# Optimization experiments

Measured on AMD Instinct MI355X. Metric: run time of the kernel, lower is better.

The kernel has to match this reference:

```python
import jax, jax.numpy as jnp
import numpy as np

EMBED = 2048
N_HEAD = 32
N_KV = 8
HEAD_DIM = 64
GROUP = N_HEAD // N_KV


def _rope_tables(seq_len, head_dim):
    inv_freq = 1.0 / (10000.0 ** (jnp.arange(0, head_dim, 2, dtype=jnp.float32) / head_dim))
    ang = jnp.arange(seq_len, dtype=jnp.float32)[:, None] * inv_freq[None, :]  # [S, D/2]
    ang = jnp.concatenate([ang, ang], axis=-1)  # [S, D]
    return jnp.cos(ang), jnp.sin(ang)


def apply_rope(x, cos, sin, offset=0):
    # x: [B, H, S, D]
    S, D = x.shape[2], x.shape[3]
    x1, x2 = x[..., : D // 2], x[..., D // 2 :]
    c = cos[offset : offset + S][None, None]
    s = sin[offset : offset + S][None, None]
    rotated = jnp.concatenate([-x2, x1], axis=-1)
    return (x * c + rotated * s).astype(x.dtype)


def setup_inputs() -> dict:
    key = jax.random.key(0)
    kx, kq, kk, kv, ko = jax.random.split(key, 5)
    B, S = 2, 2048
    x = jax.random.normal(kx, (B, S, EMBED), dtype=jnp.float32)
    mask = jnp.triu(jnp.ones((S, S), dtype=bool), k=1)  # causal: True = masked
    cos, sin = _rope_tables(S, HEAD_DIM)
    std = 0.02
    Wq = jax.random.normal(kq, (EMBED, EMBED), dtype=jnp.float32) * std
    Wk = jax.random.normal(kk, (EMBED, N_KV * HEAD_DIM), dtype=jnp.float32) * std
    Wv = jax.random.normal(kv, (EMBED, N_KV * HEAD_DIM), dtype=jnp.float32) * std
    Wo = jax.random.normal(ko, (EMBED, EMBED), dtype=jnp.float32) * std
    return {"x": x, "mask": mask, "cos": cos, "sin": sin,
            "Wq": Wq, "Wk": Wk, "Wv": Wv, "Wo": Wo}


def reference(x, mask, cos, sin, Wq, Wk, Wv, Wo):
    B, S, E = x.shape
    # projections (no bias)
    q = (x @ Wq).reshape(B, S, N_HEAD, HEAD_DIM).transpose(0, 2, 1, 3)  # [B,H,S,D]
    k = (x @ Wk).reshape(B, S, N_KV, HEAD_DIM).transpose(0, 2, 1, 3)    # [B,G,S,D]
    v = (x @ Wv).reshape(B, S, N_KV, HEAD_DIM).transpose(0, 2, 1, 3)    # [B,G,S,D]
    q = apply_rope(q, cos, sin, offset=0)
    k = apply_rope(k, cos, sin, offset=0)
    next_k, next_v = k, v  # kv cache to return
    # GQA: head h uses kv group h // GROUP; avoid repeat_interleave via reshape
    qg = q.reshape(B, N_KV, GROUP, S, HEAD_DIM)
    scores = jnp.einsum('bgjsd,bgtd->bgjst', qg, k) / np.float32(np.sqrt(HEAD_DIM))
    scores = jnp.where(mask[None, None, None], -jnp.inf, scores)
    attn = jax.nn.softmax(scores, axis=-1)
    out = jnp.einsum('bgjst,bgtd->bgjsd', attn, v)          # [B,G,group,S,D]
    out = out.reshape(B, N_HEAD, S, HEAD_DIM).transpose(0, 2, 1, 3).reshape(B, S, E)
    return out @ Wo, next_k, next_v
```

## Files before the change

kernel.cpp:

```cpp
#include <hip/hip_runtime.h>
#include <hip/hip_bf16.h>
#include <math.h>

#define NH 32
#define NKV 8
#define HD 64
#define B_ 2
#define S_ 2048
#define E_ 2048
#define M_ 4096

typedef unsigned short ushort_t;
typedef __attribute__((ext_vector_type(8))) short short8;
typedef __attribute__((ext_vector_type(4))) short short4v;
typedef __attribute__((ext_vector_type(4))) float floatx4;

__device__ inline unsigned short f2bf(float f) {
  unsigned int u = __float_as_uint(f);
  return (unsigned short)((u + 0x7FFFu + ((u >> 16) & 1u)) >> 16);
}

__device__ inline float fexp2(float x) {
  float r;
  asm("v_exp_f32 %0, %1" : "=v"(r) : "v"(x));
  return r;
}

__device__ inline void ld_lds16(const void* g, void* l) {
  __builtin_amdgcn_global_load_lds((__attribute__((address_space(1))) void*)g,
                                   (__attribute__((address_space(3))) void*)l, 16, 0, 0);
}

__global__ __launch_bounds__(256) void cast_x(const float* __restrict__ x,
                                              ushort_t* __restrict__ xb) {
  size_t i = ((size_t)blockIdx.x * 256 + threadIdx.x) * 8;
  float4 a = *(const float4*)(x + i);
  float4 b = *(const float4*)(x + i + 4);
  short8 o;
  o[0] = (short)f2bf(a.x); o[1] = (short)f2bf(a.y);
  o[2] = (short)f2bf(a.z); o[3] = (short)f2bf(a.w);
  o[4] = (short)f2bf(b.x); o[5] = (short)f2bf(b.y);
  o[6] = (short)f2bf(b.z); o[7] = (short)f2bf(b.w);
  *(short8*)(xb + i) = o;
}

__global__ __launch_bounds__(256) void transpose_w(const float* __restrict__ in,
                                                   ushort_t* __restrict__ out,
                                                   int R, int C) {
  __shared__ float tile[32][33];
  int c0 = blockIdx.x * 32, r0 = blockIdx.y * 32;
  int x = threadIdx.x, y0 = threadIdx.y;
  for (int i = 0; i < 4; i++) {
    int r = y0 + i * 8;
    tile[r][x] = in[(size_t)(r0 + r) * C + c0 + x];
  }
  __syncthreads();
  for (int i = 0; i < 4; i++) {
    int r = y0 + i * 8;
    out[(size_t)(c0 + r) * R + r0 + x] = f2bf(tile[x][r]);
  }
}

__global__ __launch_bounds__(256) void transpose_v(const float* __restrict__ outv,
                                                   ushort_t* __restrict__ vt) {
  __shared__ float t64[64][65];
  int bg = blockIdx.y;
  int tt = blockIdx.x;
  int s0 = tt * 64;
  int tid = threadIdx.x;
  size_t ibase = (size_t)bg * S_ * HD + (size_t)s0 * HD;
  for (int i = tid; i < 1024; i += 256) {
    int sr = i >> 4, dc = (i & 15) * 4;
    float4 v = *(const float4*)(outv + ibase + (size_t)sr * HD + dc);
    t64[sr][dc] = v.x; t64[sr][dc + 1] = v.y; t64[sr][dc + 2] = v.z; t64[sr][dc + 3] = v.w;
  }
  __syncthreads();
  size_t obase = ((size_t)bg * 32 + tt) * 4096;
  for (int i = tid; i < 512; i += 256) {
    int d = i >> 3, ss = (i & 7) * 8;
    short8 o;
#pragma unroll
    for (int e = 0; e < 8; e++) o[e] = (short)f2bf(t64[ss + e][d]);
    *(short8*)(vt + obase + d * 64 + (ss ^ ((d & 7) << 3))) = o;
  }
}

__global__ __launch_bounds__(256) void gemm_qkv(const ushort_t* __restrict__ xb,
                                                const ushort_t* __restrict__ WT,
                                                ushort_t* __restrict__ qbf,
                                                float* __restrict__ outk,
                                                ushort_t* __restrict__ kbf,
                                                float* __restrict__ outv,
                                                const float* __restrict__ cosP,
                                                const float* __restrict__ sinP) {
  __shared__ __align__(16) ushort_t As[128][32];
  __shared__ __align__(16) ushort_t Bs[128][32];
  const int K = 2048;
  int tid = threadIdx.x;
  int m0 = blockIdx.y * 128, n0 = blockIdx.x * 128;
  int w = tid >> 6, lane = tid & 63;
  int wm = (w >> 1) * 64, wn = (w & 1) * 64;
  int lr = lane & 15, quad = lane >> 4;
  int srow = lane >> 2, soff = (lane & 3) * 16;
  floatx4 acc[4][4] = {};
  for (int kt = 0; kt < 64; kt++) {
    __syncthreads();
#pragma unroll
    for (int j = 0; j < 2; j++) {
      int r = j * 64 + w * 16;
      ld_lds16((const char*)(xb + (size_t)(m0 + r + srow) * K) + kt * 64 + soff,
               (char*)As + r * 64);
      ld_lds16((const char*)(WT + (size_t)(n0 + r + srow) * K) + kt * 64 + soff,
               (char*)Bs + r * 64);
    }
    __syncthreads();
    short8 af[4], bf[4];
#pragma unroll
    for (int i = 0; i < 4; i++) af[i] = *(const short8*)(&As[wm + i * 16 + lr][quad * 8]);
#pragma unroll
    for (int j = 0; j < 4; j++) bf[j] = *(const short8*)(&Bs[wn + j * 16 + lr][quad * 8]);
#pragma unroll
    for (int i = 0; i < 4; i++)
#pragma unroll
      for (int j = 0; j < 4; j++)
        acc[i][j] = __builtin_amdgcn_mfma_f32_16x16x32_bf16(af[i], bf[j], acc[i][j], 0, 0, 0);
  }
  if (n0 < 2048) {
    const float QS = 0.125f * 1.4426950408889634f;
#pragma unroll
    for (int i = 0; i < 4; i++)
#pragma unroll
      for (int j = 0; j < 2; j++) {
        int d = j * 16 + lr;
#pragma unroll
        for (int r = 0; r < 4; r++) {
          int row = m0 + wm + i * 16 + quad * 4 + r;
          int s = row & (S_ - 1);
          float c = cosP[s * 64 + d], sn = sinP[s * 64 + d];
          float x1 = acc[i][j][r], x2 = acc[i][j + 2][r];
          size_t o = (size_t)row * 2048 + n0 + wn + d;
          qbf[o] = f2bf((x1 * c - x2 * sn) * QS);
          qbf[o + 32] = f2bf((x2 * c + x1 * sn) * QS);
        }
      }
  } else if (n0 < 2560) {
    int h = (n0 - 2048 + wn) >> 6;
#pragma unroll
    for (int i = 0; i < 4; i++)
#pragma unroll
      for (int j = 0; j < 2; j++) {
        int d = j * 16 + lr;
#pragma unroll
        for (int r = 0; r < 4; r++) {
          int row = m0 + wm + i * 16 + quad * 4 + r;
          int s = row & (S_ - 1), b = row >> 11;
          float c = cosP[s * 64 + d], sn = sinP[s * 64 + d];
          float x1 = acc[i][j][r], x2 = acc[i][j + 2][r];
          float y1 = x1 * c - x2 * sn, y2 = x2 * c + x1 * sn;
          size_t rowb = ((size_t)(b * NKV + h) * S_ + s) * 64;
          int xr = (s & 7) << 3;
          outk[rowb + d] = y1; outk[rowb + d + 32] = y2;
          kbf[rowb + (d ^ xr)] = f2bf(y1);
          kbf[rowb + ((d + 32) ^ xr)] = f2bf(y2);
        }
      }
  } else {
    int cv0 = n0 - 2560 + wn;
    int h = cv0 >> 6;
#pragma unroll
    for (int i = 0; i < 4; i++)
#pragma unroll
      for (int j = 0; j < 4; j++) {
        int d = j * 16 + lr;
#pragma unroll
        for (int r = 0; r < 4; r++) {
          int row = m0 + wm + i * 16 + quad * 4 + r;
          int s = row & (S_ - 1), b = row >> 11;
          outv[((size_t)(b * NKV + h) * S_ + s) * 64 + d] = acc[i][j][r];
        }
      }
  }
}

__global__ __launch_bounds__(256) void gemm_o(const ushort_t* __restrict__ ctx,
                                              const ushort_t* __restrict__ WoT,
                                              float* __restrict__ y) {
  __shared__ __align__(16) ushort_t As[128][32];
  __shared__ __align__(16) ushort_t Bs[128][32];
  const int K = 2048, N = 2048;
  int tid = threadIdx.x;
  int m0 = blockIdx.y * 128, n0 = blockIdx.x * 128;
  int w = tid >> 6, lane = tid & 63;
  int wm = (w >> 1) * 64, wn = (w & 1) * 64;
  int lr = lane & 15, quad = lane >> 4;
  int srow = lane >> 2, soff = (lane & 3) * 16;
  floatx4 acc[4][4] = {};
  for (int kt = 0; kt < 64; kt++) {
    __syncthreads();
#pragma unroll
    for (int j = 0; j < 2; j++) {
      int r = j * 64 + w * 16;
      ld_lds16((const char*)(ctx + (size_t)(m0 + r + srow) * K) + kt * 64 + soff,
               (char*)As + r * 64);
      ld_lds16((const char*)(WoT + (size_t)(n0 + r + srow) * K) + kt * 64 + soff,
               (char*)Bs + r * 64);
    }
    __syncthreads();
    short8 af[4], bf[4];
#pragma unroll
    for (int i = 0; i < 4; i++) af[i] = *(const short8*)(&As[wm + i * 16 + lr][quad * 8]);
#pragma unroll
    for (int j = 0; j < 4; j++) bf[j] = *(const short8*)(&Bs[wn + j * 16 + lr][quad * 8]);
#pragma unroll
    for (int i = 0; i < 4; i++)
#pragma unroll
      for (int j = 0; j < 4; j++)
        acc[i][j] = __builtin_amdgcn_mfma_f32_16x16x32_bf16(af[i], bf[j], acc[i][j], 0, 0, 0);
  }
#pragma unroll
  for (int i = 0; i < 4; i++)
#pragma unroll
    for (int j = 0; j < 4; j++) {
      int row = m0 + wm + i * 16 + quad * 4;
      int col = n0 + wn + j * 16 + lr;
#pragma unroll
      for (int r = 0; r < 4; r++)
        y[(size_t)(row + r) * N + col] = acc[i][j][r];
    }
}

__global__ __launch_bounds__(256, 4) void attn2(ushort_t* __restrict__ q,
                                                const ushort_t* __restrict__ k,
                                                const ushort_t* __restrict__ vt) {
  __shared__ __align__(16) ushort_t KV[2][2][64][64];
  __shared__ __align__(16) ushort_t Ps[4][16][64];
  int bh = blockIdx.x;
  int qt = 31 - blockIdx.y;
  int b = bh >> 5, h = bh & 31, g = h >> 2;
  int tid = threadIdx.x;
  int w = tid >> 6, lane = tid & 63;
  int lr = lane & 15, quad = lane >> 4;

  int qg = qt * 64 + w * 16 + lr;
  short8 aq0, aq1;
  {
    const ushort_t* qp = q + ((size_t)(b * S_ + qg) * NH + h) * HD;
    aq0 = *(const short8*)(qp + quad * 8);
    aq1 = *(const short8*)(qp + 32 + quad * 8);
  }
  floatx4 od[4] = {};
  float mi = -INFINITY, li = 0.f;

  const char* ksrc = (const char*)(k + (size_t)(b * NKV + g) * S_ * HD) + w * 2048 + lane * 16;
  const char* vsrc = (const char*)(vt + (size_t)(b * NKV + g) * S_ * HD) + w * 2048 + lane * 16;
  char* dB = (char*)&KV[0][0][0][0] + w * 2048;

  int sw = (lr & 7) << 4;
  int ro0 = (quad * 16) ^ sw;
  int ro1 = (64 + quad * 16) ^ sw;
  char* Pw = (char*)&Ps[0][0][0] + w * 2048;

  ld_lds16(ksrc, dB);
  ld_lds16(ksrc + 1024, dB + 1024);
  ld_lds16(vsrc, dB + 8192);
  ld_lds16(vsrc + 1024, dB + 8192 + 1024);
  asm volatile("s_waitcnt vmcnt(0)" ::: "memory");
  __syncthreads();

  int cur = 0;
  for (int t = 0; t <= qt; t++) {
    if (t < qt) {
      const char* kn = ksrc + (size_t)(t + 1) * 8192;
      const char* vn = vsrc + (size_t)(t + 1) * 8192;
      char* d = dB + (cur ^ 1) * 16384;
      ld_lds16(kn, d); ld_lds16(kn + 1024, d + 1024);
      ld_lds16(vn, d + 8192); ld_lds16(vn + 1024, d + 8192 + 1024);
    }
    const char* Kb = (const char*)&KV[cur][0][0][0];
    const char* Vb = (const char*)&KV[cur][1][0][0];
    floatx4 sc[4];
#pragma unroll
    for (int kn = 0; kn < 4; kn++) {
      short8 a0 = *(const short8*)(Kb + (kn * 16 + lr) * 128 + ro0);
      short8 a1 = *(const short8*)(Kb + (kn * 16 + lr) * 128 + ro1);
      floatx4 c = {};
      c = __builtin_amdgcn_mfma_f32_16x16x32_bf16(a0, aq0, c, 0, 0, 0);
      c = __builtin_amdgcn_mfma_f32_16x16x32_bf16(a1, aq1, c, 0, 0, 0);
      sc[kn] = c;
    }
    float pv[16];
#pragma unroll
    for (int kn = 0; kn < 4; kn++)
#pragma unroll
      for (int r = 0; r < 4; r++) pv[kn * 4 + r] = sc[kn][r];
    if (t == qt) {
#pragma unroll
      for (int e = 0; e < 16; e++) {
        int kg = t * 64 + (e >> 2) * 16 + quad * 4 + (e & 3);
        if (kg > qg) pv[e] = -INFINITY;
      }
    }
    float mx = pv[0];
#pragma unroll
    for (int e = 1; e < 16; e++) mx = fmaxf(mx, pv[e]);
    mx = fmaxf(mx, __shfl_xor(mx, 16));
    mx = fmaxf(mx, __shfl_xor(mx, 32));
    if (__any(mx > mi + 11.5f)) {
      float mn = fmaxf(mi, mx);
      float al = fexp2(mi - mn);
      li *= al;
#pragma unroll
      for (int dn = 0; dn < 4; dn++) {
        od[dn][0] *= al; od[dn][1] *= al; od[dn][2] *= al; od[dn][3] *= al;
      }
      mi = mn;
    }
    float ps = 0.f;
#pragma unroll
    for (int e = 0; e < 16; e++) {
      pv[e] = fexp2(pv[e] - mi);
      ps += pv[e];
    }
    ps += __shfl_xor(ps, 16);
    ps += __shfl_xor(ps, 32);
    li += ps;
#pragma unroll
    for (int kn = 0; kn < 4; kn++) {
      unsigned int u0, u1;
      asm("v_cvt_pk_bf16_f32 %0, %1, %2" : "=v"(u0) : "v"(pv[kn * 4 + 0]), "v"(pv[kn * 4 + 1]));
      asm("v_cvt_pk_bf16_f32 %0, %1, %2" : "=v"(u1) : "v"(pv[kn * 4 + 2]), "v"(pv[kn * 4 + 3]));
      uint2 uu; uu.x = u0; uu.y = u1;
      *(uint2*)(Pw + lr * 128 + ((kn * 32 + quad * 8) ^ sw)) = uu;
    }
    short8 pb0 = *(const short8*)(Pw + lr * 128 + ro0);
    short8 pb1 = *(const short8*)(Pw + lr * 128 + ro1);
#pragma unroll
    for (int dn = 0; dn < 4; dn++) {
      short8 va = *(const short8*)(Vb + (dn * 16 + lr) * 128 + ro0);
      short8 vb = *(const short8*)(Vb + (dn * 16 + lr) * 128 + ro1);
      od[dn] = __builtin_amdgcn_mfma_f32_16x16x32_bf16(va, pb0, od[dn], 0, 0, 0);
      od[dn] = __builtin_amdgcn_mfma_f32_16x16x32_bf16(vb, pb1, od[dn], 0, 0, 0);
    }
    asm volatile("s_waitcnt vmcnt(0)" ::: "memory");
    __syncthreads();
    cur ^= 1;
  }
  float inv = 1.f / li;
  ushort_t* outp = q + ((size_t)(b * S_ + qg) * NH + h) * HD;
#pragma unroll
  for (int dn = 0; dn < 4; dn++) {
    short4v u;
    u[0] = (short)f2bf(od[dn][0] * inv); u[1] = (short)f2bf(od[dn][1] * inv);
    u[2] = (short)f2bf(od[dn][2] * inv); u[3] = (short)f2bf(od[dn][3] * inv);
    *(short4v*)(outp + dn * 16 + quad * 4) = u;
  }
}

extern "C" void kernel_launch(void* const* d_in, const int* in_sizes, int n_in,
                              void* d_out, int out_size, void* d_ws, size_t ws_size,
                              hipStream_t stream) {
  const float* x = (const float*)d_in[0];
  const float* cosT = (const float*)d_in[2];
  const float* sinT = (const float*)d_in[3];
  const float* Wq = (const float*)d_in[4];
  const float* Wk = (const float*)d_in[5];
  const float* Wv = (const float*)d_in[6];
  const float* Wo = (const float*)d_in[7];

  char* ws = (char*)d_ws;
  ushort_t* WT = (ushort_t*)(ws);
  ushort_t* WoT = (ushort_t*)(ws + 12582912);
  ushort_t* xb = (ushort_t*)(ws + 20971520);
  ushort_t* qbf = (ushort_t*)(ws + 37748736);
  ushort_t* kbf = (ushort_t*)(ws + 54525952);
  ushort_t* vt = (ushort_t*)(ws + 58720256);

  float* y = (float*)d_out;
  float* outk = y + (size_t)M_ * E_;
  float* outv = outk + (size_t)B_ * NKV * S_ * HD;

  cast_x<<<dim3(4096), 256, 0, stream>>>(x, xb);
  transpose_w<<<dim3(64, 64), dim3(32, 8), 0, stream>>>(Wq, WT, 2048, 2048);
  transpose_w<<<dim3(16, 64), dim3(32, 8), 0, stream>>>(Wk, WT + 2048 * 2048, 2048, 512);
  transpose_w<<<dim3(16, 64), dim3(32, 8), 0, stream>>>(Wv, WT + 2560 * 2048, 2048, 512);
  transpose_w<<<dim3(64, 64), dim3(32, 8), 0, stream>>>(Wo, WoT, 2048, 2048);

  gemm_qkv<<<dim3(24, 32), 256, 0, stream>>>(xb, WT, qbf, outk, kbf, outv, cosT, sinT);
  transpose_v<<<dim3(32, 16), 256, 0, stream>>>(outv, vt);

  attn2<<<dim3(64, 32), 256, 0, stream>>>(qbf, kbf, vt);

  gemm_o<<<dim3(16, 32), 256, 0, stream>>>(qbf, WoT, y);
}
```

Baseline: 360.6 us.

## Double-buffer GEMM tiles with wider K step, XOR-swizzled LDS, and block swizzle

```diff
diff --git a/kernel.cpp b/kernel.cpp
--- a/kernel.cpp
+++ b/kernel.cpp
@@ -85,6 +85,73 @@
   }
 }
 
+__device__ __forceinline__ void gemm128_core(const ushort_t* __restrict__ Ag,
+                                             const ushort_t* __restrict__ Bg,
+                                             floatx4 (&acc)[4][4]) {
+  __shared__ __align__(16) ushort_t As[2][128][64];
+  __shared__ __align__(16) ushort_t Bs[2][128][64];
+  int tid = threadIdx.x;
+  int w = tid >> 6, lane = tid & 63;
+  int wm = (w >> 1) * 64, wn = (w & 1) * 64;
+  int lr = lane & 15, quad = lane >> 4;
+  int sx = lr & 7;
+  char* Asb = (char*)As;
+  char* Bsb = (char*)Bs;
+
+  size_t so[4];
+#pragma unroll
+  for (int s = 0; s < 4; s++)
+    so[s] = (size_t)(w * 32 + s * 8 + (lane >> 3)) * 4096 + (size_t)(((lane & 7) ^ (lane >> 3)) * 16);
+  const char* abase = (const char*)Ag;
+  const char* bbase = (const char*)Bg;
+
+#define STAGE128(buf, kt)                                          \
+  do {                                                             \
+    size_t ko = (size_t)(kt) * 128;                                \
+    char* Ad = Asb + (buf) * 16384 + w * 4096;                     \
+    char* Bd = Bsb + (buf) * 16384 + w * 4096;                     \
+    _Pragma("unroll") for (int s = 0; s < 4; s++) {                \
+      ld_lds16(abase + so[s] + ko, Ad + s * 1024);                 \
+      ld_lds16(bbase + so[s] + ko, Bd + s * 1024);                 \
+    }                                                              \
+  } while (0)
+
+  STAGE128(0, 0);
+  __syncthreads();
+
+  int cur = 0;
+  for (int kt = 0; kt < 32; kt++) {
+    if (kt < 31) STAGE128(cur ^ 1, kt + 1);
+    const char* Ab = Asb + cur * 16384;
+    const char* Bb = Bsb + cur * 16384;
+    short8 af[4][2], bfr[4][2];
+#pragma unroll
+    for (int i = 0; i < 4; i++) {
+      size_t rb = (size_t)(wm + i * 16 + lr) * 128;
+#pragma unroll
+      for (int ks = 0; ks < 2; ks++)
+        af[i][ks] = *(const short8*)(Ab + rb + (((ks * 4 + quad) ^ sx) << 4));
+    }
+#pragma unroll
+    for (int j = 0; j < 4; j++) {
+      size_t rb = (size_t)(wn + j * 16 + lr) * 128;
+#pragma unroll
+      for (int ks = 0; ks < 2; ks++)
+        bfr[j][ks] = *(const short8*)(Bb + rb + (((ks * 4 + quad) ^ sx) << 4));
+    }
+#pragma unroll
+    for (int i = 0; i < 4; i++)
+#pragma unroll
+      for (int j = 0; j < 4; j++) {
+        acc[i][j] = __builtin_amdgcn_mfma_f32_16x16x32_bf16(af[i][0], bfr[j][0], acc[i][j], 0, 0, 0);
+        acc[i][j] = __builtin_amdgcn_mfma_f32_16x16x32_bf16(af[i][1], bfr[j][1], acc[i][j], 0, 0, 0);
+      }
+    __syncthreads();
+    cur ^= 1;
+  }
+#undef STAGE128
+}
+
 __global__ __launch_bounds__(256) void gemm_qkv(const ushort_t* __restrict__ xb,
                                                 const ushort_t* __restrict__ WT,
                                                 ushort_t* __restrict__ qbf,
@@ -93,38 +160,17 @@
                                                 float* __restrict__ outv,
                                                 const float* __restrict__ cosP,
                                                 const float* __restrict__ sinP) {
-  __shared__ __align__(16) ushort_t As[128][32];
-  __shared__ __align__(16) ushort_t Bs[128][32];
-  const int K = 2048;
+  int o = blockIdx.y * 24 + blockIdx.x;
+  int swz = (o & 7) * 96 + (o >> 3);
+  int n0 = (swz % 24) * 128, m0 = (swz / 24) * 128;
   int tid = threadIdx.x;
-  int m0 = blockIdx.y * 128, n0 = blockIdx.x * 128;
   int w = tid >> 6, lane = tid & 63;
   int wm = (w >> 1) * 64, wn = (w & 1) * 64;
   int lr = lane & 15, quad = lane >> 4;
-  int srow = lane >> 2, soff = (lane & 3) * 16;
+
   floatx4 acc[4][4] = {};
-  for (int kt = 0; kt < 64; kt++) {
-    __syncthreads();
-#pragma unroll
-    for (int j = 0; j < 2; j++) {
-      int r = j * 64 + w * 16;
-      ld_lds16((const char*)(xb + (size_t)(m0 + r + srow) * K) + kt * 64 + soff,
-               (char*)As + r * 64);
-      ld_lds16((const char*)(WT + (size_t)(n0 + r + srow) * K) + kt * 64 + soff,
-               (char*)Bs + r * 64);
-    }
-    __syncthreads();
-    short8 af[4], bf[4];
-#pragma unroll
-    for (int i = 0; i < 4; i++) af[i] = *(const short8*)(&As[wm + i * 16 + lr][quad * 8]);
-#pragma unroll
-    for (int j = 0; j < 4; j++) bf[j] = *(const short8*)(&Bs[wn + j * 16 + lr][quad * 8]);
-#pragma unroll
-    for (int i = 0; i < 4; i++)
-#pragma unroll
-      for (int j = 0; j < 4; j++)
-        acc[i][j] = __builtin_amdgcn_mfma_f32_16x16x32_bf16(af[i], bf[j], acc[i][j], 0, 0, 0);
-  }
+  gemm128_core(xb + (size_t)m0 * 2048, WT + (size_t)n0 * 2048, acc);
+
   if (n0 < 2048) {
     const float QS = 0.125f * 1.4426950408889634f;
 #pragma unroll
@@ -138,9 +184,9 @@
           int s = row & (S_ - 1);
           float c = cosP[s * 64 + d], sn = sinP[s * 64 + d];
           float x1 = acc[i][j][r], x2 = acc[i][j + 2][r];
-          size_t o = (size_t)row * 2048 + n0 + wn + d;
-          qbf[o] = f2bf((x1 * c - x2 * sn) * QS);
-          qbf[o + 32] = f2bf((x2 * c + x1 * sn) * QS);
+          size_t oo = (size_t)row * 2048 + n0 + wn + d;
+          qbf[oo] = f2bf((x1 * c - x2 * sn) * QS);
+          qbf[oo + 32] = f2bf((x2 * c + x1 * sn) * QS);
         }
       }
   } else if (n0 < 2560) {
@@ -165,8 +211,7 @@
         }
       }
   } else {
-    int cv0 = n0 - 2560 + wn;
-    int h = cv0 >> 6;
+    int h = (n0 - 2560 + wn) >> 6;
 #pragma unroll
     for (int i = 0; i < 4; i++)
 #pragma unroll
@@ -185,38 +230,17 @@
 __global__ __launch_bounds__(256) void gemm_o(const ushort_t* __restrict__ ctx,
                                               const ushort_t* __restrict__ WoT,
                                               float* __restrict__ y) {
-  __shared__ __align__(16) ushort_t As[128][32];
-  __shared__ __align__(16) ushort_t Bs[128][32];
-  const int K = 2048, N = 2048;
+  int o = blockIdx.y * 16 + blockIdx.x;
+  int swz = (o & 7) * 64 + (o >> 3);
+  int n0 = (swz % 16) * 128, m0 = (swz / 16) * 128;
   int tid = threadIdx.x;
-  int m0 = blockIdx.y * 128, n0 = blockIdx.x * 128;
   int w = tid >> 6, lane = tid & 63;
   int wm = (w >> 1) * 64, wn = (w & 1) * 64;
   int lr = lane & 15, quad = lane >> 4;
-  int srow = lane >> 2, soff = (lane & 3) * 16;
+
   floatx4 acc[4][4] = {};
-  for (int kt = 0; kt < 64; kt++) {
-    __syncthreads();
-#pragma unroll
-    for (int j = 0; j < 2; j++) {
-      int r = j * 64 + w * 16;
-      ld_lds16((const char*)(ctx + (size_t)(m0 + r + srow) * K) + kt * 64 + soff,
-               (char*)As + r * 64);
-      ld_lds16((const char*)(WoT + (size_t)(n0 + r + srow) * K) + kt * 64 + soff,
-               (char*)Bs + r * 64);
-    }
-    __syncthreads();
-    short8 af[4], bf[4];
-#pragma unroll
-    for (int i = 0; i < 4; i++) af[i] = *(const short8*)(&As[wm + i * 16 + lr][quad * 8]);
-#pragma unroll
-    for (int j = 0; j < 4; j++) bf[j] = *(const short8*)(&Bs[wn + j * 16 + lr][quad * 8]);
-#pragma unroll
-    for (int i = 0; i < 4; i++)
-#pragma unroll
-      for (int j = 0; j < 4; j++)
-        acc[i][j] = __builtin_amdgcn_mfma_f32_16x16x32_bf16(af[i], bf[j], acc[i][j], 0, 0, 0);
-  }
+  gemm128_core(ctx + (size_t)m0 * 2048, WoT + (size_t)n0 * 2048, acc);
+
 #pragma unroll
   for (int i = 0; i < 4; i++)
 #pragma unroll
@@ -225,7 +249,7 @@
       int col = n0 + wn + j * 16 + lr;
 #pragma unroll
       for (int r = 0; r < 4; r++)
-        y[(size_t)(row + r) * N + col] = acc[i][j][r];
+        y[(size_t)(row + r) * 2048 + col] = acc[i][j][r];
     }
 }
 
```

Measured after the change: 344.0 us. 1.05x faster.
